# Performance work log

Measured on AMD Instinct MI355X. Metric: run time of the kernel, lower is better.

The kernel has to match this reference:

```python
import jax, jax.numpy as jnp
import numpy as np

EMBED = 1024
HEADS = 16
HEAD_DIM = EMBED // HEADS


def setup_inputs() -> dict:
    key = jax.random.key(0)
    k1, k2, k3 = jax.random.split(key, 3)
    return {
        "hidden_states": jax.random.normal(k1, (2, 2048, EMBED), dtype=jnp.float32),
        "c_attn_w": jax.random.normal(k2, (EMBED, 3 * EMBED), dtype=jnp.float32) * 0.02,
        "c_attn_b": jnp.zeros((3 * EMBED,), dtype=jnp.float32),
        "c_proj_w": jax.random.normal(k3, (EMBED, EMBED), dtype=jnp.float32) * 0.02,
        "c_proj_b": jnp.zeros((EMBED,), dtype=jnp.float32),
    }


def reference(hidden_states, c_attn_w, c_attn_b, c_proj_w, c_proj_b):
    B, S, E = hidden_states.shape
    H, D = HEADS, HEAD_DIM
    qkv = hidden_states @ c_attn_w + c_attn_b  # [B,S,3E]
    q, k, v = jnp.split(qkv, 3, axis=-1)
    # split heads -> [B,H,S,D]
    def split_heads(t):
        return t.reshape(B, S, H, D).transpose(0, 2, 1, 3)
    q, k, v = split_heads(q), split_heads(k), split_heads(v)
    scores = jnp.einsum("bhqd,bhkd->bhqk", q, k) / jnp.asarray(D ** 0.5, q.dtype)
    causal = jnp.tril(jnp.ones((S, S), dtype=bool))[None, None]
    mask_value = jnp.finfo(scores.dtype).min
    scores = jnp.where(causal, scores, mask_value)
    attn_weights = jax.nn.softmax(scores, axis=-1)  # [B,H,S,S]
    attn_out = jnp.einsum("bhqk,bhkd->bhqd", attn_weights, v)
    attn_out = attn_out.transpose(0, 2, 1, 3).reshape(B, S, E)
    attn_out = attn_out @ c_proj_w + c_proj_b
    return attn_out, attn_weights
```

## Files before the change

### kernel.cpp

```cpp
#include <hip/hip_runtime.h>
#include <hip/hip_bf16.h>

#define EMBED 1024
#define HEADS 16
#define HEAD_DIM 64
#define BATCH 2
#define SEQ 2048
#define MROWS (BATCH*SEQ)
#define NQKV  (3*EMBED)

typedef __attribute__((ext_vector_type(8))) short short8;
typedef __attribute__((ext_vector_type(4))) float float4v;

static __device__ __forceinline__ short f2bf(float f) {
    union { float f; unsigned u; } x; x.f = f;
    unsigned r = (x.u + 0x7FFFu + ((x.u >> 16) & 1u)) >> 16;
    return (short)r;
}

static __device__ __forceinline__ void gl_lds16(const short* g, short* l) {
    __builtin_amdgcn_global_load_lds(
        (const __attribute__((address_space(1))) void*)g,
        (__attribute__((address_space(3))) void*)l, 16, 0, 0);
}

__global__ __launch_bounds__(256) void cast_bf16_k(const float* __restrict__ in,
                                                   short* __restrict__ out, int n8) {
    int i = blockIdx.x * 256 + threadIdx.x;
    if (i >= n8) return;
    const float4* p = (const float4*)in + (size_t)i * 2;
    float4 a = p[0], b = p[1];
    short8 o;
    o[0] = f2bf(a.x); o[1] = f2bf(a.y); o[2] = f2bf(a.z); o[3] = f2bf(a.w);
    o[4] = f2bf(b.x); o[5] = f2bf(b.y); o[6] = f2bf(b.z); o[7] = f2bf(b.w);
    *((short8*)out + i) = o;
}

__global__ __launch_bounds__(256) void transpose_cast_k(const float* __restrict__ W,
                                                        short* __restrict__ Wt,
                                                        int K, int N) {
    __shared__ float tile[32][33];
    int tx = threadIdx.x & 31, ty = threadIdx.x >> 5;
    int n0 = blockIdx.x * 32, k0 = blockIdx.y * 32;
#pragma unroll
    for (int i = 0; i < 4; i++)
        tile[ty + i * 8][tx] = W[(size_t)(k0 + ty + i * 8) * N + n0 + tx];
    __syncthreads();
#pragma unroll
    for (int i = 0; i < 4; i++)
        Wt[(size_t)(n0 + ty + i * 8) * K + k0 + tx] = f2bf(tile[tx][ty + i * 8]);
}

__global__ __launch_bounds__(256) void gemm128_k(const short* __restrict__ A,
                                                 const short* __restrict__ Bt,
                                                 const float* __restrict__ bias,
                                                 float* __restrict__ outF,
                                                 short* __restrict__ outB,
                                                 int M, int N, int K) {
    __shared__ __align__(16) short As[128 * 32];
    __shared__ __align__(16) short Bs[128 * 32];
    const int tid = threadIdx.x;
    const int wave = tid >> 6, lane = tid & 63, quad = lane >> 4, l16 = lane & 15;
    const int wm = wave >> 1, wn = wave & 1;
    const int m0 = blockIdx.x * 128, n0 = blockIdx.y * 128;

    float4v acc[4][4];
#pragma unroll
    for (int mi = 0; mi < 4; mi++)
#pragma unroll
        for (int ni = 0; ni < 4; ni++) acc[mi][ni] = (float4v){0.f, 0.f, 0.f, 0.f};

    const int rA0 = wave * 32 + (lane >> 2), cA = (lane & 3) * 8;
    const size_t arow0 = (size_t)(m0 + rA0) * K, arow1 = (size_t)(m0 + rA0 + 16) * K;
    const size_t brow0 = (size_t)(n0 + rA0) * K, brow1 = (size_t)(n0 + rA0 + 16) * K;
    short* ldsA0 = &As[(wave * 128 + lane) * 8];
    short* ldsA1 = &As[(wave * 128 + 64 + lane) * 8];
    short* ldsB0 = &Bs[(wave * 128 + lane) * 8];
    short* ldsB1 = &Bs[(wave * 128 + 64 + lane) * 8];

    for (int k0 = 0; k0 < K; k0 += 32) {
        __syncthreads();
        gl_lds16(A + arow0 + k0 + cA, ldsA0);
        gl_lds16(A + arow1 + k0 + cA, ldsA1);
        gl_lds16(Bt + brow0 + k0 + cA, ldsB0);
        gl_lds16(Bt + brow1 + k0 + cA, ldsB1);
        __syncthreads();
        short8 a[4], b[4];
#pragma unroll
        for (int mi = 0; mi < 4; mi++)
            a[mi] = *(const short8*)&As[(wm * 64 + mi * 16 + l16) * 32 + quad * 8];
#pragma unroll
        for (int ni = 0; ni < 4; ni++)
            b[ni] = *(const short8*)&Bs[(wn * 64 + ni * 16 + l16) * 32 + quad * 8];
#pragma unroll
        for (int mi = 0; mi < 4; mi++)
#pragma unroll
            for (int ni = 0; ni < 4; ni++)
                acc[mi][ni] = __builtin_amdgcn_mfma_f32_16x16x32_bf16(a[mi], b[ni], acc[mi][ni], 0, 0, 0);
    }

#pragma unroll
    for (int ni = 0; ni < 4; ni++) {
        int col = n0 + wn * 64 + ni * 16 + l16;
        float bv = bias ? bias[col] : 0.f;
#pragma unroll
        for (int mi = 0; mi < 4; mi++) {
            int row = m0 + wm * 64 + mi * 16 + quad * 4;
            if (outF) {
#pragma unroll
                for (int i = 0; i < 4; i++)
                    outF[(size_t)(row + i) * N + col] = acc[mi][ni][i] + bv;
            } else {
#pragma unroll
                for (int i = 0; i < 4; i++)
                    outB[(size_t)(row + i) * N + col] = f2bf(acc[mi][ni][i] + bv);
            }
        }
    }
}

__global__ __launch_bounds__(256) void attn_k(const short* __restrict__ qkv,
                                              float* __restrict__ wout,
                                              short* __restrict__ aheads) {
    __shared__ __align__(16) short Qs[2][64 * 32];
    __shared__ __align__(16) short Ks[2][64 * 32];
    __shared__ __align__(16) short Vt[64 * 72];
    __shared__ __align__(16) short Ps[64 * 72];

    const int tid = threadIdx.x;
    const int wave = tid >> 6, lane = tid & 63, quad = lane >> 4, l16 = lane & 15;
    const int bh = blockIdx.x & 31;
    const int b = bh >> 4, h = bh & 15;
    const int qt = 31 - (blockIdx.x >> 5);
    const int q0 = qt * 64;
    const int nch = qt + 1;

    const short* qbase = qkv + (size_t)(b * SEQ) * NQKV + h * 64;
    const short* kbase = qbase + EMBED;
    const short* vbase = qbase + 2 * EMBED;
    float* wrow = wout + ((size_t)bh * SEQ + q0) * SEQ;

    {
        const int r = lane >> 2, c = (lane & 3) * 8;
        gl_lds16(qbase + (size_t)(q0 + wave * 16 + r) * NQKV + c,
                 &Qs[0][(wave * 64 + lane) * 8]);
        gl_lds16(qbase + (size_t)(q0 + wave * 16 + r) * NQKV + 32 + c,
                 &Qs[1][(wave * 64 + lane) * 8]);
    }
    __syncthreads();
    short8 aq0 = *(const short8*)&Qs[0][(wave * 16 + l16) * 32 + quad * 8];
    short8 aq1 = *(const short8*)&Qs[1][(wave * 16 + l16) * 32 + quad * 8];

    const int kr = lane >> 2, kc16 = (lane & 3) * 8;
    const int vkp = (tid & 31) * 2, vd8 = (tid >> 5) * 8;

    float m[4], l[4];
#pragma unroll
    for (int i = 0; i < 4; i++) { m[i] = -1e30f; l[i] = 0.f; }

    for (int c = 0; c < nch; c++) {
        const int kc = c * 64;
        __syncthreads();
        gl_lds16(kbase + (size_t)(kc + wave * 16 + kr) * NQKV + kc16,
                 &Ks[0][(wave * 64 + lane) * 8]);
        gl_lds16(kbase + (size_t)(kc + wave * 16 + kr) * NQKV + 32 + kc16,
                 &Ks[1][(wave * 64 + lane) * 8]);
        __syncthreads();
        float4v sc[4];
#pragma unroll
        for (int kg = 0; kg < 4; kg++) {
            short8 bk0 = *(const short8*)&Ks[0][(kg * 16 + l16) * 32 + quad * 8];
            short8 bk1 = *(const short8*)&Ks[1][(kg * 16 + l16) * 32 + quad * 8];
            float4v s = (float4v){0.f, 0.f, 0.f, 0.f};
            s = __builtin_amdgcn_mfma_f32_16x16x32_bf16(aq0, bk0, s, 0, 0, 0);
            s = __builtin_amdgcn_mfma_f32_16x16x32_bf16(aq1, bk1, s, 0, 0, 0);
            sc[kg] = s;
        }
        if (c < qt) {
#pragma unroll
            for (int i = 0; i < 4; i++) {
                float mx = m[i];
#pragma unroll
                for (int kg = 0; kg < 4; kg++) mx = fmaxf(mx, sc[kg][i] * 0.125f);
                float s0 = 0.f;
#pragma unroll
                for (int kg = 0; kg < 4; kg++) s0 += __expf(sc[kg][i] * 0.125f - mx);
                l[i] = l[i] * __expf(m[i] - mx) + s0;
                m[i] = mx;
            }
        } else {
#pragma unroll
            for (int i = 0; i < 4; i++) {
                int qrl = wave * 16 + quad * 4 + i;
                float mx = m[i];
#pragma unroll
                for (int kg = 0; kg < 4; kg++)
                    if (kg * 16 + l16 <= qrl) mx = fmaxf(mx, sc[kg][i] * 0.125f);
                float s0 = 0.f;
#pragma unroll
                for (int kg = 0; kg < 4; kg++)
                    if (kg * 16 + l16 <= qrl) s0 += __expf(sc[kg][i] * 0.125f - mx);
                l[i] = l[i] * __expf(m[i] - mx) + s0;
                m[i] = mx;
            }
        }
    }
    float Mi[4], Li[4];
#pragma unroll
    for (int i = 0; i < 4; i++) {
        float mm = m[i], ll = l[i];
#pragma unroll
        for (int off = 1; off <= 8; off <<= 1) {
            float mo = __shfl_xor(mm, off);
            float lo = __shfl_xor(ll, off);
            float mn = fmaxf(mm, mo);
            ll = ll * __expf(mm - mn) + lo * __expf(mo - mn);
            mm = mn;
        }
        Mi[i] = mm; Li[i] = 1.0f / ll;
    }

    float4v oacc[4];
#pragma unroll
    for (int dg = 0; dg < 4; dg++) oacc[dg] = (float4v){0.f, 0.f, 0.f, 0.f};

    for (int c = 0; c < nch; c++) {
        const int kc = c * 64;
        __syncthreads();
        gl_lds16(kbase + (size_t)(kc + wave * 16 + kr) * NQKV + kc16,
                 &Ks[0][(wave * 64 + lane) * 8]);
        gl_lds16(kbase + (size_t)(kc + wave * 16 + kr) * NQKV + 32 + kc16,
                 &Ks[1][(wave * 64 + lane) * 8]);
        {
            short8 va = *(const short8*)&vbase[(size_t)(kc + vkp) * NQKV + vd8];
            short8 vb = *(const short8*)&vbase[(size_t)(kc + vkp + 1) * NQKV + vd8];
#pragma unroll
            for (int i = 0; i < 8; i++) {
                short2 pk; pk.x = va[i]; pk.y = vb[i];
                *(short2*)&Vt[(vd8 + i) * 72 + vkp] = pk;
            }
        }
        __syncthreads();
        float4v sc[4];
#pragma unroll
        for (int kg = 0; kg < 4; kg++) {
            short8 bk0 = *(const short8*)&Ks[0][(kg * 16 + l16) * 32 + quad * 8];
            short8 bk1 = *(const short8*)&Ks[1][(kg * 16 + l16) * 32 + quad * 8];
            float4v s = (float4v){0.f, 0.f, 0.f, 0.f};
            s = __builtin_amdgcn_mfma_f32_16x16x32_bf16(aq0, bk0, s, 0, 0, 0);
            s = __builtin_amdgcn_mfma_f32_16x16x32_bf16(aq1, bk1, s, 0, 0, 0);
            sc[kg] = s;
        }
        const bool diag = (c == qt);
#pragma unroll
        for (int i = 0; i < 4; i++) {
            int lrow = wave * 16 + quad * 4 + i;
            float* wr = wrow + (size_t)lrow * SEQ + kc;
#pragma unroll
            for (int kg = 0; kg < 4; kg++) {
                float p = 0.f;
                if (!diag || (kg * 16 + l16 <= lrow))
                    p = __expf(sc[kg][i] * 0.125f - Mi[i]) * Li[i];
                wr[kg * 16 + l16] = p;
                Ps[lrow * 72 + kg * 16 + l16] = f2bf(p);
            }
        }
#pragma unroll
        for (int kh = 0; kh < 2; kh++) {
            short8 ap = *(const short8*)&Ps[(wave * 16 + l16) * 72 + kh * 32 + quad * 8];
#pragma unroll
            for (int dg = 0; dg < 4; dg++) {
                short8 bv = *(const short8*)&Vt[(dg * 16 + l16) * 72 + kh * 32 + quad * 8];
                oacc[dg] = __builtin_amdgcn_mfma_f32_16x16x32_bf16(ap, bv, oacc[dg], 0, 0, 0);
            }
        }
    }

    const int kend = (qt + 1) * 64;
    if (kend < SEQ) {
        float4 z4 = make_float4(0.f, 0.f, 0.f, 0.f);
        for (int row = 0; row < 64; row++) {
            float* p = wrow + (size_t)row * SEQ;
            for (int cc = kend + tid * 4; cc < SEQ; cc += 1024)
                *(float4*)(p + cc) = z4;
        }
    }

    short* obase = aheads + (size_t)(b * SEQ) * EMBED + h * 64;
#pragma unroll
    for (int i = 0; i < 4; i++) {
        int qg = q0 + wave * 16 + quad * 4 + i;
#pragma unroll
        for (int dg = 0; dg < 4; dg++)
            obase[(size_t)qg * EMBED + dg * 16 + l16] = f2bf(oacc[dg][i]);
    }
}

extern "C" void kernel_launch(void* const* d_in, const int* in_sizes, int n_in,
                              void* d_out, int out_size, void* d_ws, size_t ws_size,
                              hipStream_t stream) {
    const float* hidden = (const float*)d_in[0];
    const float* attn_w = (const float*)d_in[1];
    const float* attn_b = (const float*)d_in[2];
    const float* proj_w = (const float*)d_in[3];
    const float* proj_b = (const float*)d_in[4];

    float* out      = (float*)d_out;
    float* attn_out = out;
    float* weights  = out + (size_t)MROWS * EMBED;

    char* ws = (char*)d_ws;
    short* hid_b   = (short*)(ws);
    short* wqkv_t  = (short*)(ws + 8388608);
    short* wproj_t = (short*)(ws + 14680064);
    short* qkv     = (short*)(ws + 16777216);
    short* aheads  = (short*)(ws + 41943040);

    cast_bf16_k<<<dim3((MROWS * EMBED / 8 + 255) / 256), 256, 0, stream>>>(
        hidden, hid_b, MROWS * EMBED / 8);
    transpose_cast_k<<<dim3(NQKV / 32, EMBED / 32), 256, 0, stream>>>(
        attn_w, wqkv_t, EMBED, NQKV);
    transpose_cast_k<<<dim3(EMBED / 32, EMBED / 32), 256, 0, stream>>>(
        proj_w, wproj_t, EMBED, EMBED);
    gemm128_k<<<dim3(MROWS / 128, NQKV / 128), 256, 0, stream>>>(
        hid_b, wqkv_t, attn_b, nullptr, qkv, MROWS, NQKV, EMBED);
    attn_k<<<dim3(BATCH * HEADS * (SEQ / 64)), 256, 0, stream>>>(
        qkv, weights, aheads);
    gemm128_k<<<dim3(MROWS / 128, EMBED / 128), 256, 0, stream>>>(
        aheads, wproj_t, proj_b, attn_out, nullptr, MROWS, EMBED, EMBED);
}
```

Before: 722.1 us.

## Swap MFMA operand order for row-contiguous outputs, fold Q scaling into QKV GEMM

Swaps the A/B operands of every MFMA so each lane holds four consecutive columns of one row, which allows 16-byte float4 and 8-byte short4 vector stores in the GEMM epilogue, the attention weight writes and the head-output writes. The 1/sqrt(D) scale is folded into the QKV GEMM epilogue for the Q columns, removing the per-score multiplies in attention. In the attention statistics pass, Q and K are now read directly from global memory instead of being staged in LDS, which removes that pass's barriers. The row max/sum state drops to one value per lane, combined across quads with shuffles. Risks are uncoalesced direct global K reads and changed rounding, since Q is scaled before the bf16 cast.

```diff
diff --git a/kernel.cpp b/kernel.cpp
--- a/kernel.cpp
+++ b/kernel.cpp
@@ -10,6 +10,7 @@
 #define NQKV  (3*EMBED)
 
 typedef __attribute__((ext_vector_type(8))) short short8;
+typedef __attribute__((ext_vector_type(4))) short short4v;
 typedef __attribute__((ext_vector_type(4))) float float4v;
 
 static __device__ __forceinline__ short f2bf(float f) {
@@ -56,7 +57,7 @@
                                                  const float* __restrict__ bias,
                                                  float* __restrict__ outF,
                                                  short* __restrict__ outB,
-                                                 int M, int N, int K) {
+                                                 int M, int N, int K, int qscale_cols) {
     __shared__ __align__(16) short As[128 * 32];
     __shared__ __align__(16) short Bs[128 * 32];
     const int tid = threadIdx.x;
@@ -66,9 +67,9 @@
 
     float4v acc[4][4];
 #pragma unroll
-    for (int mi = 0; mi < 4; mi++)
-#pragma unroll
-        for (int ni = 0; ni < 4; ni++) acc[mi][ni] = (float4v){0.f, 0.f, 0.f, 0.f};
+    for (int ni = 0; ni < 4; ni++)
+#pragma unroll
+        for (int mi = 0; mi < 4; mi++) acc[ni][mi] = (float4v){0.f, 0.f, 0.f, 0.f};
 
     const int rA0 = wave * 32 + (lane >> 2), cA = (lane & 3) * 8;
     const size_t arow0 = (size_t)(m0 + rA0) * K, arow1 = (size_t)(m0 + rA0 + 16) * K;
@@ -93,27 +94,31 @@
         for (int ni = 0; ni < 4; ni++)
             b[ni] = *(const short8*)&Bs[(wn * 64 + ni * 16 + l16) * 32 + quad * 8];
 #pragma unroll
-        for (int mi = 0; mi < 4; mi++)
-#pragma unroll
-            for (int ni = 0; ni < 4; ni++)
-                acc[mi][ni] = __builtin_amdgcn_mfma_f32_16x16x32_bf16(a[mi], b[ni], acc[mi][ni], 0, 0, 0);
+        for (int ni = 0; ni < 4; ni++)
+#pragma unroll
+            for (int mi = 0; mi < 4; mi++)
+                acc[ni][mi] = __builtin_amdgcn_mfma_f32_16x16x32_bf16(b[ni], a[mi], acc[ni][mi], 0, 0, 0);
     }
 
 #pragma unroll
     for (int ni = 0; ni < 4; ni++) {
-        int col = n0 + wn * 64 + ni * 16 + l16;
-        float bv = bias ? bias[col] : 0.f;
+        const int col = n0 + wn * 64 + ni * 16 + quad * 4;
+        float4v bv4 = (float4v){0.f, 0.f, 0.f, 0.f};
+        if (bias) bv4 = *(const float4v*)&bias[col];
+        const float scl = (col < qscale_cols) ? 0.125f : 1.0f;
 #pragma unroll
         for (int mi = 0; mi < 4; mi++) {
-            int row = m0 + wm * 64 + mi * 16 + quad * 4;
+            const int row = m0 + wm * 64 + mi * 16 + l16;
+            float4v v = acc[ni][mi];
+#pragma unroll
+            for (int i = 0; i < 4; i++) v[i] = (v[i] + bv4[i]) * scl;
             if (outF) {
-#pragma unroll
-                for (int i = 0; i < 4; i++)
-                    outF[(size_t)(row + i) * N + col] = acc[mi][ni][i] + bv;
+                *(float4v*)&outF[(size_t)row * N + col] = v;
             } else {
-#pragma unroll
-                for (int i = 0; i < 4; i++)
-                    outB[(size_t)(row + i) * N + col] = f2bf(acc[mi][ni][i] + bv);
+                short4v s4;
+#pragma unroll
+                for (int i = 0; i < 4; i++) s4[i] = f2bf(v[i]);
+                *(short4v*)&outB[(size_t)row * N + col] = s4;
             }
         }
     }
@@ -122,7 +127,6 @@
 __global__ __launch_bounds__(256) void attn_k(const short* __restrict__ qkv,
                                               float* __restrict__ wout,
                                               short* __restrict__ aheads) {
-    __shared__ __align__(16) short Qs[2][64 * 32];
     __shared__ __align__(16) short Ks[2][64 * 32];
     __shared__ __align__(16) short Vt[64 * 72];
     __shared__ __align__(16) short Ps[64 * 72];
@@ -140,31 +144,89 @@
     const short* vbase = qbase + 2 * EMBED;
     float* wrow = wout + ((size_t)bh * SEQ + q0) * SEQ;
 
-    {
-        const int r = lane >> 2, c = (lane & 3) * 8;
-        gl_lds16(qbase + (size_t)(q0 + wave * 16 + r) * NQKV + c,
-                 &Qs[0][(wave * 64 + lane) * 8]);
-        gl_lds16(qbase + (size_t)(q0 + wave * 16 + r) * NQKV + 32 + c,
-                 &Qs[1][(wave * 64 + lane) * 8]);
-    }
-    __syncthreads();
-    short8 aq0 = *(const short8*)&Qs[0][(wave * 16 + l16) * 32 + quad * 8];
-    short8 aq1 = *(const short8*)&Qs[1][(wave * 16 + l16) * 32 + quad * 8];
+    const int qloc = wave * 16 + l16;
+    const int klo = quad * 4;
+
+    const short* qrow = qbase + (size_t)(q0 + qloc) * NQKV;
+    const short8 aq0 = *(const short8*)(qrow + quad * 8);
+    const short8 aq1 = *(const short8*)(qrow + 32 + quad * 8);
+
+    float m = -1e30f, l = 0.f;
+
+    for (int c = 0; c < nch; c++) {
+        const int kc = c * 64;
+        float4v sc[4];
+#pragma unroll
+        for (int kg = 0; kg < 4; kg++) {
+            const short* kr = kbase + (size_t)(kc + kg * 16 + l16) * NQKV;
+            short8 bk0 = *(const short8*)(kr + quad * 8);
+            short8 bk1 = *(const short8*)(kr + 32 + quad * 8);
+            float4v s = (float4v){0.f, 0.f, 0.f, 0.f};
+            s = __builtin_amdgcn_mfma_f32_16x16x32_bf16(bk0, aq0, s, 0, 0, 0);
+            s = __builtin_amdgcn_mfma_f32_16x16x32_bf16(bk1, aq1, s, 0, 0, 0);
+            sc[kg] = s;
+        }
+        if (c < qt) {
+            float mx = m;
+#pragma unroll
+            for (int kg = 0; kg < 4; kg++)
+#pragma unroll
+                for (int i = 0; i < 4; i++) mx = fmaxf(mx, sc[kg][i]);
+            float s0 = 0.f;
+#pragma unroll
+            for (int kg = 0; kg < 4; kg++)
+#pragma unroll
+                for (int i = 0; i < 4; i++) s0 += __expf(sc[kg][i] - mx);
+            l = l * __expf(m - mx) + s0;
+            m = mx;
+        } else {
+            float mx = m;
+#pragma unroll
+            for (int kg = 0; kg < 4; kg++)
+#pragma unroll
+                for (int i = 0; i < 4; i++)
+                    if (kg * 16 + klo + i <= qloc) mx = fmaxf(mx, sc[kg][i]);
+            float s0 = 0.f;
+#pragma unroll
+            for (int kg = 0; kg < 4; kg++)
+#pragma unroll
+                for (int i = 0; i < 4; i++)
+                    s0 += (kg * 16 + klo + i <= qloc) ? __expf(sc[kg][i] - mx) : 0.f;
+            l = l * __expf(m - mx) + s0;
+            m = mx;
+        }
+    }
+#pragma unroll
+    for (int off = 16; off <= 32; off <<= 1) {
+        float mo = __shfl_xor(m, off);
+        float lo = __shfl_xor(l, off);
+        float mn = fmaxf(m, mo);
+        l = l * __expf(m - mn) + lo * __expf(mo - mn);
+        m = mn;
+    }
+    const float Mi = m, Li = 1.0f / l;
+
+    float4v oacc[4];
+#pragma unroll
+    for (int dg = 0; dg < 4; dg++) oacc[dg] = (float4v){0.f, 0.f, 0.f, 0.f};
 
     const int kr = lane >> 2, kc16 = (lane & 3) * 8;
     const int vkp = (tid & 31) * 2, vd8 = (tid >> 5) * 8;
 
-    float m[4], l[4];
-#pragma unroll
-    for (int i = 0; i < 4; i++) { m[i] = -1e30f; l[i] = 0.f; }
-
     for (int c = 0; c < nch; c++) {
         const int kc = c * 64;
+        short8 va = *(const short8*)&vbase[(size_t)(kc + vkp) * NQKV + vd8];
+        short8 vb = *(const short8*)&vbase[(size_t)(kc + vkp + 1) * NQKV + vd8];
         __syncthreads();
         gl_lds16(kbase + (size_t)(kc + wave * 16 + kr) * NQKV + kc16,
                  &Ks[0][(wave * 64 + lane) * 8]);
         gl_lds16(kbase + (size_t)(kc + wave * 16 + kr) * NQKV + 32 + kc16,
                  &Ks[1][(wave * 64 + lane) * 8]);
+#pragma unroll
+        for (int i = 0; i < 8; i++) {
+            short2 pk; pk.x = va[i]; pk.y = vb[i];
+            *(short2*)&Vt[(vd8 + i) * 72 + vkp] = pk;
+        }
         __syncthreads();
         float4v sc[4];
 #pragma unroll
@@ -172,106 +234,34 @@
             short8 bk0 = *(const short8*)&Ks[0][(kg * 16 + l16) * 32 + quad * 8];
             short8 bk1 = *(const short8*)&Ks[1][(kg * 16 + l16) * 32 + quad * 8];
             float4v s = (float4v){0.f, 0.f, 0.f, 0.f};
-            s = __builtin_amdgcn_mfma_f32_16x16x32_bf16(aq0, bk0, s, 0, 0, 0);
-            s = __builtin_amdgcn_mfma_f32_16x16x32_bf16(aq1, bk1, s, 0, 0, 0);
+            s = __builtin_amdgcn_mfma_f32_16x16x32_bf16(bk0, aq0, s, 0, 0, 0);
+            s = __builtin_amdgcn_mfma_f32_16x16x32_bf16(bk1, aq1, s, 0, 0, 0);
             sc[kg] = s;
         }
-        if (c < qt) {
+        const bool diag = (c == qt);
+        float* wr = wrow + (size_t)qloc * SEQ + kc;
+#pragma unroll
+        for (int kg = 0; kg < 4; kg++) {
+            float4v w4;
+            short4v p4;
 #pragma unroll
             for (int i = 0; i < 4; i++) {
-                float mx = m[i];
-#pragma unroll
-                for (int kg = 0; kg < 4; kg++) mx = fmaxf(mx, sc[kg][i] * 0.125f);
-                float s0 = 0.f;
-#pragma unroll
-                for (int kg = 0; kg < 4; kg++) s0 += __expf(sc[kg][i] * 0.125f - mx);
-                l[i] = l[i] * __expf(m[i] - mx) + s0;
-                m[i] = mx;
+                float p = 0.f;
+                if (!diag || (kg * 16 + klo + i <= qloc))
+                    p = __expf(sc[kg][i] - Mi) * Li;
+                w4[i] = p;
+                p4[i] = f2bf(p);
             }
-        } else {
-#pragma unroll
-            for (int i = 0; i < 4; i++) {
-                int qrl = wave * 16 + quad * 4 + i;
-                float mx = m[i];
-#pragma unroll
-                for (int kg = 0; kg < 4; kg++)
-                    if (kg * 16 + l16 <= qrl) mx = fmaxf(mx, sc[kg][i] * 0.125f);
-                float s0 = 0.f;
-#pragma unroll
-                for (int kg = 0; kg < 4; kg++)
-                    if (kg * 16 + l16 <= qrl) s0 += __expf(sc[kg][i] * 0.125f - mx);
-                l[i] = l[i] * __expf(m[i] - mx) + s0;
-                m[i] = mx;
-            }
-        }
-    }
-    float Mi[4], Li[4];
-#pragma unroll
-    for (int i = 0; i < 4; i++) {
-        float mm = m[i], ll = l[i];
-#pragma unroll
-        for (int off = 1; off <= 8; off <<= 1) {
-            float mo = __shfl_xor(mm, off);
-            float lo = __shfl_xor(ll, off);
-            float mn = fmaxf(mm, mo);
-            ll = ll * __expf(mm - mn) + lo * __expf(mo - mn);
-            mm = mn;
-        }
-        Mi[i] = mm; Li[i] = 1.0f / ll;
-    }
-
-    float4v oacc[4];
-#pragma unroll
-    for (int dg = 0; dg < 4; dg++) oacc[dg] = (float4v){0.f, 0.f, 0.f, 0.f};
-
-    for (int c = 0; c < nch; c++) {
-        const int kc = c * 64;
-        __syncthreads();
-        gl_lds16(kbase + (size_t)(kc + wave * 16 + kr) * NQKV + kc16,
-                 &Ks[0][(wave * 64 + lane) * 8]);
-        gl_lds16(kbase + (size_t)(kc + wave * 16 + kr) * NQKV + 32 + kc16,
-                 &Ks[1][(wave * 64 + lane) * 8]);
-        {
-            short8 va = *(const short8*)&vbase[(size_t)(kc + vkp) * NQKV + vd8];
-            short8 vb = *(const short8*)&vbase[(size_t)(kc + vkp + 1) * NQKV + vd8];
-#pragma unroll
-            for (int i = 0; i < 8; i++) {
-                short2 pk; pk.x = va[i]; pk.y = vb[i];
-                *(short2*)&Vt[(vd8 + i) * 72 + vkp] = pk;
-            }
-        }
-        __syncthreads();
-        float4v sc[4];
-#pragma unroll
-        for (int kg = 0; kg < 4; kg++) {
-            short8 bk0 = *(const short8*)&Ks[0][(kg * 16 + l16) * 32 + quad * 8];
-            short8 bk1 = *(const short8*)&Ks[1][(kg * 16 + l16) * 32 + quad * 8];
-            float4v s = (float4v){0.f, 0.f, 0.f, 0.f};
-            s = __builtin_amdgcn_mfma_f32_16x16x32_bf16(aq0, bk0, s, 0, 0, 0);
-            s = __builtin_amdgcn_mfma_f32_16x16x32_bf16(aq1, bk1, s, 0, 0, 0);
-            sc[kg] = s;
-        }
-        const bool diag = (c == qt);
-#pragma unroll
-        for (int i = 0; i < 4; i++) {
-            int lrow = wave * 16 + quad * 4 + i;
-            float* wr = wrow + (size_t)lrow * SEQ + kc;
-#pragma unroll
-            for (int kg = 0; kg < 4; kg++) {
-                float p = 0.f;
-                if (!diag || (kg * 16 + l16 <= lrow))
-                    p = __expf(sc[kg][i] * 0.125f - Mi[i]) * Li[i];
-                wr[kg * 16 + l16] = p;
-                Ps[lrow * 72 + kg * 16 + l16] = f2bf(p);
-            }
+            *(float4v*)(wr + kg * 16 + klo) = w4;
+            *(short4v*)&Ps[qloc * 72 + kg * 16 + klo] = p4;
         }
 #pragma unroll
         for (int kh = 0; kh < 2; kh++) {
-            short8 ap = *(const short8*)&Ps[(wave * 16 + l16) * 72 + kh * 32 + quad * 8];
+            short8 ap = *(const short8*)&Ps[qloc * 72 + kh * 32 + quad * 8];
 #pragma unroll
             for (int dg = 0; dg < 4; dg++) {
                 short8 bv = *(const short8*)&Vt[(dg * 16 + l16) * 72 + kh * 32 + quad * 8];
-                oacc[dg] = __builtin_amdgcn_mfma_f32_16x16x32_bf16(ap, bv, oacc[dg], 0, 0, 0);
+                oacc[dg] = __builtin_amdgcn_mfma_f32_16x16x32_bf16(bv, ap, oacc[dg], 0, 0, 0);
             }
         }
     }
@@ -287,12 +277,13 @@
     }
 
     short* obase = aheads + (size_t)(b * SEQ) * EMBED + h * 64;
-#pragma unroll
-    for (int i = 0; i < 4; i++) {
-        int qg = q0 + wave * 16 + quad * 4 + i;
-#pragma unroll
-        for (int dg = 0; dg < 4; dg++)
-            obase[(size_t)qg * EMBED + dg * 16 + l16] = f2bf(oacc[dg][i]);
+    const size_t orow = (size_t)(q0 + qloc) * EMBED;
+#pragma unroll
+    for (int dg = 0; dg < 4; dg++) {
+        short4v o4;
+#pragma unroll
+        for (int i = 0; i < 4; i++) o4[i] = f2bf(oacc[dg][i]);
+        *(short4v*)&obase[orow + dg * 16 + klo] = o4;
     }
 }
 
@@ -323,9 +314,9 @@
     transpose_cast_k<<<dim3(EMBED / 32, EMBED / 32), 256, 0, stream>>>(
         proj_w, wproj_t, EMBED, EMBED);
     gemm128_k<<<dim3(MROWS / 128, NQKV / 128), 256, 0, stream>>>(
-        hid_b, wqkv_t, attn_b, nullptr, qkv, MROWS, NQKV, EMBED);
+        hid_b, wqkv_t, attn_b, nullptr, qkv, MROWS, NQKV, EMBED, EMBED);
     attn_k<<<dim3(BATCH * HEADS * (SEQ / 64)), 256, 0, stream>>>(
         qkv, weights, aheads);
     gemm128_k<<<dim3(MROWS / 128, EMBED / 128), 256, 0, stream>>>(
-        aheads, wproj_t, proj_b, attn_out, nullptr, MROWS, EMBED, EMBED);
-}
+        aheads, wproj_t, proj_b, attn_out, nullptr, MROWS, EMBED, EMBED, 0);
+}
```

After: 770.2 us. +6.7%, slower.
